# Performance work log

Measured on AMD Instinct MI355X. Metric: run time of the kernel, lower is better.

The kernel has to match this reference:

```python
import jax, jax.numpy as jnp
import numpy as np
from jax import lax

BSZ, BEAM, VOCAB, D = 32, 4, 50257, 1024
MAXLEN = 64
L = MAXLEN + 2            # tokens buffer length (bos + maxlen+1 slots)
SLEN = MAXLEN + 1         # scores buffer length
PAD, EOS, UNK = 1, 2, 3
TEMP = 1.0
LEN_PEN = 1.0
UNK_PEN = 0.0
NEG = jnp.float32(-1e9)   # stand-in for -inf (safe for grads)


def setup_inputs() -> dict:
    key = jax.random.key(0)
    k1, k2, k3 = jax.random.split(key, 3)
    # 0.02 scaling keeps logits in a realistic range
    emb = jax.random.normal(k1, (VOCAB, D), jnp.float32) * 0.02
    W_out = jax.random.normal(k2, (D, VOCAB), jnp.float32) * 0.02
    pos_emb = jax.random.normal(k3, (SLEN, D), jnp.float32) * 0.02
    return {"emb": emb, "W_out": W_out, "pos_emb": pos_emb}


def _decode(emb, W_out, pos_emb, tokens, step):
    # stand-in decoder: prev-token embedding + pos embedding -> vocab logits
    prev = lax.dynamic_index_in_dim(tokens, step, axis=1, keepdims=False)  # [bbsz]
    h = emb[prev] + pos_emb[step]                                          # [bbsz, D]
    lp = jax.nn.log_softmax((h @ W_out) / TEMP, axis=-1)                   # [bbsz, V]
    lp = lp.at[:, PAD].set(NEG)
    lp = lp.at[:, UNK].add(-UNK_PEN)
    return lp


def _beam_search(emb, W_out, pos_emb):
    bbsz = BSZ * BEAM
    tokens = jnp.full((bbsz, L), PAD, jnp.int32).at[:, 0].set(EOS)
    scores = jnp.zeros((bbsz, SLEN), jnp.float32)
    fin_tok = jnp.zeros((BSZ, BEAM, L), jnp.int32)
    fin_sc = jnp.full((BSZ, BEAM), NEG, jnp.float32)
    offsets = jnp.arange(2 * BEAM, dtype=jnp.int32)
    colL = jnp.arange(L)
    colS = jnp.arange(SLEN)
    barange = jnp.arange(BEAM)

    def step_fn(carry, step):
        tokens, scores, fin_tok, fin_sc = carry
        lp = _decode(emb, W_out, pos_emb, tokens, step).reshape(BSZ, BEAM, VOCAB)
        prev_sc = lax.dynamic_index_in_dim(scores, jnp.maximum(step - 1, 0), axis=1, keepdims=False)
        prev_sc = jnp.where(step == 0, 0.0, prev_sc).reshape(BSZ, BEAM)
        cum = lp + prev_sc[:, :, None]
        # step 0: only the first beam participates (fairseq BeamSearch.step)
        cum = jnp.where((step == 0) & (barange[None, :, None] > 0), NEG, cum)
        cand_sc, cand_flat = lax.top_k(cum.reshape(BSZ, BEAM * VOCAB), 2 * BEAM)
        cand_beam = cand_flat // VOCAB       # [BSZ, 2*BEAM]
        cand_tok = cand_flat % VOCAB
        tokens3 = tokens.reshape(BSZ, BEAM, L)
        # --- finalize eos hypotheses from the first BEAM candidates ---
        eos_mask_b = cand_tok[:, :BEAM] == EOS
        eos_norm = jnp.where(eos_mask_b, cand_sc[:, :BEAM] / (step + 1.0) ** LEN_PEN, NEG)
        eos_tok = jnp.take_along_axis(tokens3, cand_beam[:, :BEAM, None], axis=1)
        eos_tok = jnp.where(colL[None, None, :] == step + 1, EOS, eos_tok)
        all_sc = jnp.concatenate([fin_sc, eos_norm], axis=1)
        all_tok = jnp.concatenate([fin_tok, eos_tok], axis=1)
        fin_sc, sel = lax.top_k(all_sc, BEAM)
        fin_tok = jnp.take_along_axis(all_tok, sel[:, :, None], axis=1)
        # --- pick BEAM active (non-eos) hypotheses (smallest active_mask) ---
        eos_mask = (cand_tok == EOS).astype(jnp.int32)
        amask = eos_mask * (2 * BEAM) + offsets[None, :]
        _, active = lax.top_k(-amask, BEAM)
        act_beam = jnp.take_along_axis(cand_beam, active, axis=1)
        act_tok = jnp.take_along_axis(cand_tok, active, axis=1)
        act_sc = jnp.take_along_axis(cand_sc, active, axis=1)
        # --- reorder beams, append new token / score ---
        tokens3 = jnp.take_along_axis(tokens3, act_beam[:, :, None], axis=1)
        tokens3 = jnp.where(colL[None, None, :] == step + 1, act_tok[:, :, None], tokens3)
        scores3 = jnp.take_along_axis(scores.reshape(BSZ, BEAM, SLEN), act_beam[:, :, None], axis=1)
        scores3 = jnp.where(colS[None, None, :] == step, act_sc[:, :, None], scores3)
        return (tokens3.reshape(bbsz, L), scores3.reshape(bbsz, SLEN), fin_tok, fin_sc), None

    carry = (tokens, scores, fin_tok, fin_sc)
    (tokens, scores, fin_tok, fin_sc), _ = lax.scan(step_fn, carry, jnp.arange(MAXLEN))
    # --- final step: force EOS on every surviving beam (step == maxlen) ---
    lp = _decode(emb, W_out, pos_emb, tokens, MAXLEN)
    eos_sc = (scores[:, MAXLEN - 1] + lp[:, EOS]).reshape(BSZ, BEAM) / (MAXLEN + 1.0) ** LEN_PEN
    tokens3 = tokens.reshape(BSZ, BEAM, L)
    eos_tok = jnp.where(jnp.arange(L)[None, None, :] == MAXLEN + 1, EOS, tokens3)
    all_sc = jnp.concatenate([fin_sc, eos_sc], axis=1)
    all_tok = jnp.concatenate([fin_tok, eos_tok], axis=1)
    fin_sc, sel = lax.top_k(all_sc, BEAM)
    fin_tok = jnp.take_along_axis(all_tok, sel[:, :, None], axis=1)
    return fin_tok, fin_sc


def reference(emb, W_out, pos_emb):
    # returns (finalized tokens [BSZ, BEAM, L] int32, normalized scores [BSZ, BEAM] f32)
    return _beam_search(emb, W_out, pos_emb)
```

## Files before the change

kernel.cpp:

```cpp
#include <hip/hip_runtime.h>
#include <cstdint>
#include <cstddef>

#define VOCAB_N 50257
#define NPAD    50304
#define DIM     1024
#define BSZ_N   32
#define BEAM_N  4
#define BB      128
#define L_N     66
#define SLEN_N  65
#define MAXLEN_N 64
#define PAD_T   1
#define EOS_T   2
#define NEGV    (-1e9f)
#define SENTV   (-3.402823466e38f)
#define PW_BLOCK 128

typedef unsigned long long u64;
typedef __attribute__((ext_vector_type(8))) _Float16 f16x8;
typedef __attribute__((ext_vector_type(4))) _Float16 f16x4;
typedef __attribute__((ext_vector_type(4))) float f32x4;

__device__ __constant__ int QLO[4] = {0, 12560, 25128, 37688};
__device__ __constant__ int QHI[4] = {12560, 25128, 37688, 50257};

struct PWTree {
    int nleaf, nint, maxlev, root;
    int lstart[256], lnum[256], lslot[256];
    int eL[256], eR[256], eD[256];
    int lvl[32];
};

constexpr PWTree build_tree(int start, int n0) {
    PWTree t{};
    int fs[64] = {}, fn[64] = {}, fstt[64] = {}, fls[64] = {}, fll[64] = {};
    int tL[256] = {}, tR[256] = {}, tD[256] = {}, tLev[256] = {};
    int sp = 0, lc = 0, nc = 0, cnt = 0;
    fs[0] = start; fn[0] = n0; fstt[0] = 0; sp = 1;
    int retslot = -1, retlev = 0;
    while (sp > 0) {
        const int n = fn[sp - 1], s = fs[sp - 1], st = fstt[sp - 1];
        if (n <= PW_BLOCK) {
            t.lstart[lc] = s; t.lnum[lc] = n; t.lslot[lc] = cnt;
            retslot = cnt; retlev = 0; ++cnt; ++lc; --sp; continue;
        }
        int L = (n >> 1); L -= (L & 7);
        if (st == 0)      { fstt[sp - 1] = 1; fs[sp] = s;     fn[sp] = L;     fstt[sp] = 0; ++sp; }
        else if (st == 1) { fls[sp - 1] = retslot; fll[sp - 1] = retlev; fstt[sp - 1] = 2;
                            fs[sp] = s + L; fn[sp] = n - L; fstt[sp] = 0; ++sp; }
        else {
            const int lv = (fll[sp - 1] > retlev ? fll[sp - 1] : retlev) + 1;
            tL[nc] = fls[sp - 1]; tR[nc] = retslot; tD[nc] = cnt; tLev[nc] = lv;
            retslot = cnt; retlev = lv; ++cnt; ++nc; --sp;
        }
    }
    int maxlev = 0;
    for (int j = 0; j < nc; ++j) if (tLev[j] > maxlev) maxlev = tLev[j];
    int cl[40] = {};
    for (int j = 0; j < nc; ++j) cl[tLev[j]]++;
    int acc = 0;
    for (int v = 1; v <= maxlev; ++v) { t.lvl[v] = acc; acc += cl[v]; }
    t.lvl[maxlev + 1] = acc;
    int pos[40] = {};
    for (int v = 1; v <= maxlev; ++v) pos[v] = t.lvl[v];
    for (int j = 0; j < nc; ++j) {
        const int v = tLev[j]; const int p = pos[v]++;
        t.eL[p] = tL[j]; t.eR[p] = tR[j]; t.eD[p] = tD[j];
    }
    t.nleaf = lc; t.nint = nc; t.maxlev = maxlev; t.root = retslot;
    return t;
}

__device__ constexpr PWTree g_q0 = build_tree(0, 12560);
__device__ constexpr PWTree g_q1 = build_tree(12560, 12568);
__device__ constexpr PWTree g_q2 = build_tree(25128, 12560);
__device__ constexpr PWTree g_q3 = build_tree(37688, 12569);

__device__ __forceinline__ unsigned sortable_f32(float x) {
    unsigned u = __float_as_uint(x);
    return (u & 0x80000000u) ? ~u : (u | 0x80000000u);
}
__device__ __forceinline__ float unsort_f32(unsigned s) {
    unsigned u = (s & 0x80000000u) ? (s & 0x7fffffffu) : ~s;
    return __uint_as_float(u);
}

__global__ void k_init(int* __restrict__ tokens, float* __restrict__ scores,
                       int* __restrict__ fin_tok, float* __restrict__ fin_sc,
                       unsigned* __restrict__ rmax_u) {
    int i = blockIdx.x * blockDim.x + threadIdx.x;
    int st = gridDim.x * blockDim.x;
    for (int k = i; k < BB * L_N; k += st) tokens[k] = ((k % L_N) == 0) ? EOS_T : PAD_T;
    for (int k = i; k < BB * SLEN_N; k += st) scores[k] = 0.f;
    for (int k = i; k < BB * L_N; k += st) fin_tok[k] = 0;
    for (int k = i; k < BB; k += st) { fin_sc[k] = NEGV; rmax_u[k] = 0u; }
}

__device__ __forceinline__ void split2(float x, _Float16& h0, _Float16& h1) {
    const float xs = x * 4096.f;
    h0 = (_Float16)xs;
    const float r = xs - (float)h0;
    h1 = (_Float16)r;
}

__global__ __launch_bounds__(256) void k_wsplit(const float* __restrict__ W,
                                                _Float16* __restrict__ Wsp) {
    __shared__ __align__(16) _Float16 B[2][64][40];
    const int bid = blockIdx.x;
    const int ct = bid % 786, kt = bid / 786;
    const int n0 = ct * 64, k0 = kt * 32;
    const int tid = threadIdx.x;
    const int c = tid & 63, kk = tid >> 6;
#pragma unroll
    for (int j = 0; j < 8; ++j) {
        const int k = kk * 8 + j;
        float wv = 0.f;
        if (n0 + c < VOCAB_N) wv = W[(size_t)(k0 + k) * VOCAB_N + n0 + c];
        _Float16 b0, b1;
        split2(wv, b0, b1);
        B[0][c][k] = b0; B[1][c][k] = b1;
    }
    __syncthreads();
    const int g = tid & 3, cc = (tid >> 2) & 63;
#pragma unroll
    for (int p = 0; p < 2; ++p)
        *(f16x8*)&Wsp[((size_t)p * NPAD + n0 + cc) * 1024 + k0 + g * 8] =
            *(const f16x8*)&B[p][cc][g * 8];
}

__global__ __launch_bounds__(256) void k_hsplit(const float* __restrict__ emb,
                                                const float* __restrict__ pos_emb,
                                                const int* __restrict__ tokens,
                                                _Float16* __restrict__ Hsp, int step) {
    const int row = blockIdx.x;
    const int tid = threadIdx.x;
    const int tok = tokens[row * L_N + step];
    const float4 e = *(const float4*)(emb + (size_t)tok * DIM + tid * 4);
    const float4 p = *(const float4*)(pos_emb + (size_t)step * DIM + tid * 4);
    const float hv[4] = {e.x + p.x, e.y + p.y, e.z + p.z, e.w + p.w};
    f16x4 o0, o1;
#pragma unroll
    for (int d = 0; d < 4; ++d) {
        _Float16 a0, a1;
        split2(hv[d], a0, a1);
        o0[d] = a0; o1[d] = a1;
    }
    *(f16x4*)&Hsp[(size_t)0 * 131072 + row * 1024 + tid * 4] = o0;
    *(f16x4*)&Hsp[(size_t)1 * 131072 + row * 1024 + tid * 4] = o1;
}

__global__ __launch_bounds__(512) void k_gemm_fast(const _Float16* __restrict__ Wsp,
                                                   const _Float16* __restrict__ Hsp,
                                                   float* __restrict__ logits,
                                                   unsigned* __restrict__ rmax_u) {
    __shared__ __align__(16) _Float16 Ha[2][128][40];
    __shared__ __align__(16) _Float16 Wb[2][128][40];
    __shared__ unsigned smax[128];
    const int tid = threadIdx.x;
    const int n0 = blockIdx.x * 128;
    const int lane = tid & 63, wid = tid >> 6;
    const int la = lane & 15, g = lane >> 4;
    const int wr = wid >> 1, wc = wid & 1;
    const int sg = tid & 3, sidx = (tid >> 2) & 127;

    if (tid < 128) smax[tid] = 0u;

    f32x4 acc[2][4];
#pragma unroll
    for (int mf = 0; mf < 2; ++mf)
#pragma unroll
        for (int nf = 0; nf < 4; ++nf)
#pragma unroll
            for (int j = 0; j < 4; ++j) acc[mf][nf][j] = 0.f;

    const _Float16* H0 = Hsp;
    const _Float16* H1 = Hsp + 131072;
    const _Float16* W0 = Wsp;
    const _Float16* W1 = Wsp + (size_t)NPAD * 1024;
    const size_t hoff = (size_t)sidx * 1024 + sg * 8;
    const size_t woff = (size_t)(n0 + sidx) * 1024 + sg * 8;

    f16x8 rH0 = *(const f16x8*)&H0[hoff];
    f16x8 rH1 = *(const f16x8*)&H1[hoff];
    f16x8 rW0 = *(const f16x8*)&W0[woff];
    f16x8 rW1 = *(const f16x8*)&W1[woff];

    for (int t = 0; t < 32; ++t) {
        *(f16x8*)&Ha[0][sidx][sg * 8] = rH0;
        *(f16x8*)&Ha[1][sidx][sg * 8] = rH1;
        *(f16x8*)&Wb[0][sidx][sg * 8] = rW0;
        *(f16x8*)&Wb[1][sidx][sg * 8] = rW1;
        __syncthreads();
        if (t + 1 < 32) {
            const int k0 = (t + 1) * 32;
            rH0 = *(const f16x8*)&H0[hoff + k0];
            rH1 = *(const f16x8*)&H1[hoff + k0];
            rW0 = *(const f16x8*)&W0[woff + k0];
            rW1 = *(const f16x8*)&W1[woff + k0];
        }
        f16x8 a[2][2];
#pragma unroll
        for (int mf = 0; mf < 2; ++mf) {
            a[mf][0] = *(const f16x8*)&Ha[0][wr * 32 + mf * 16 + la][g * 8];
            a[mf][1] = *(const f16x8*)&Ha[1][wr * 32 + mf * 16 + la][g * 8];
        }
#pragma unroll
        for (int nf = 0; nf < 4; ++nf) {
            const int c = wc * 64 + nf * 16 + la;
            const f16x8 b0 = *(const f16x8*)&Wb[0][c][g * 8];
            const f16x8 b1 = *(const f16x8*)&Wb[1][c][g * 8];
#pragma unroll
            for (int mf = 0; mf < 2; ++mf) {
                f32x4 cc = acc[mf][nf];
                cc = __builtin_amdgcn_mfma_f32_16x16x32_f16(a[mf][0], b0, cc, 0, 0, 0);
                cc = __builtin_amdgcn_mfma_f32_16x16x32_f16(a[mf][0], b1, cc, 0, 0, 0);
                cc = __builtin_amdgcn_mfma_f32_16x16x32_f16(a[mf][1], b0, cc, 0, 0, 0);
                acc[mf][nf] = cc;
            }
        }
        __syncthreads();
    }

#pragma unroll
    for (int mf = 0; mf < 2; ++mf) {
        const int row = wr * 32 + mf * 16 + g * 4;
        float rmx[4] = {SENTV, SENTV, SENTV, SENTV};
#pragma unroll
        for (int nf = 0; nf < 4; ++nf) {
            const int col = n0 + wc * 64 + nf * 16 + la;
#pragma unroll
            for (int j = 0; j < 4; ++j) {
                const float v = acc[mf][nf][j] * 0x1p-24f;
                logits[(size_t)(row + j) * NPAD + col] = v;
                rmx[j] = fmaxf(rmx[j], v);
            }
        }
#pragma unroll
        for (int j = 0; j < 4; ++j) {
            float v = rmx[j];
            v = fmaxf(v, __shfl_xor(v, 1, 64));
            v = fmaxf(v, __shfl_xor(v, 2, 64));
            v = fmaxf(v, __shfl_xor(v, 4, 64));
            v = fmaxf(v, __shfl_xor(v, 8, 64));
            if (la == 0) atomicMax(&smax[row + j], sortable_f32(v));
        }
    }
    __syncthreads();
    if (tid < 128) atomicMax(&rmax_u[tid], smax[tid]);
}

#define KT 32
__global__ __launch_bounds__(512) void k_gemm_slow(const float* __restrict__ W,
                                                   const float* __restrict__ emb,
                                                   const float* __restrict__ pos_emb,
                                                   const int* __restrict__ tokens,
                                                   float* __restrict__ logits,
                                                   unsigned* __restrict__ rmax_u, int step) {
    __shared__ __align__(16) _Float16 Ha[2][128][40];
    __shared__ __align__(16) _Float16 Wb[2][128][40];
    __shared__ unsigned smax[128];
    const int tid = threadIdx.x;
    const int n0 = blockIdx.x * 128;
    const bool full = (n0 + 128 <= VOCAB_N);
    const int lane = tid & 63, wid = tid >> 6;
    const int wr = wid >> 1, wc = wid & 1;
    const int la = lane & 15, g = lane >> 4;
    const int hrow = tid & 127, hkq = tid >> 7;
    const int tokH = tokens[hrow * L_N + step];
    const float* eprow = emb + (size_t)tokH * DIM;
    const float* pprow = pos_emb + (size_t)step * DIM;
    const int wcq = tid & 31, wk = tid >> 5;

    if (tid < 128) smax[tid] = 0u;

    f32x4 acc[2][4];
#pragma unroll
    for (int mf = 0; mf < 2; ++mf)
#pragma unroll
        for (int nf = 0; nf < 4; ++nf)
#pragma unroll
            for (int j = 0; j < 4; ++j) acc[mf][nf][j] = 0.f;

    for (int k0 = 0; k0 < DIM; k0 += KT) {
#pragma unroll
        for (int d = 0; d < 4; ++d) {
            const int c = wcq + 32 * d;
#pragma unroll
            for (int qq = 0; qq < 2; ++qq) {
                const int kk = wk + 16 * qq;
                float wv = 0.f;
                if (full || (n0 + c < VOCAB_N))
                    wv = W[(size_t)(k0 + kk) * VOCAB_N + n0 + c];
                _Float16 b0, b1;
                split2(wv, b0, b1);
                Wb[0][c][kk] = b0;
                Wb[1][c][kk] = b1;
            }
        }
#pragma unroll
        for (int qq = 0; qq < 2; ++qq) {
            const int kq = hkq + 4 * qq;
            const float4 e0 = *(const float4*)(eprow + k0 + kq * 4);
            const float4 p0 = *(const float4*)(pprow + k0 + kq * 4);
            const float hv[4] = {e0.x + p0.x, e0.y + p0.y, e0.z + p0.z, e0.w + p0.w};
            f16x4 o0, o1;
#pragma unroll
            for (int d = 0; d < 4; ++d) {
                _Float16 a0, a1;
                split2(hv[d], a0, a1);
                o0[d] = a0; o1[d] = a1;
            }
            *(f16x4*)&Ha[0][hrow][kq * 4] = o0;
            *(f16x4*)&Ha[1][hrow][kq * 4] = o1;
        }
        __syncthreads();
        f16x8 af[2][2];
#pragma unroll
        for (int mf = 0; mf < 2; ++mf)
#pragma unroll
            for (int p = 0; p < 2; ++p)
                af[mf][p] = *(const f16x8*)&Ha[p][wr * 32 + mf * 16 + la][g * 8];
#pragma unroll
        for (int nf = 0; nf < 4; ++nf) {
            const int c = wc * 64 + nf * 16 + la;
            const f16x8 b0 = *(const f16x8*)&Wb[0][c][g * 8];
            const f16x8 b1 = *(const f16x8*)&Wb[1][c][g * 8];
#pragma unroll
            for (int mf = 0; mf < 2; ++mf) {
                f32x4 cc = acc[mf][nf];
                cc = __builtin_amdgcn_mfma_f32_16x16x32_f16(af[mf][0], b0, cc, 0, 0, 0);
                cc = __builtin_amdgcn_mfma_f32_16x16x32_f16(af[mf][0], b1, cc, 0, 0, 0);
                cc = __builtin_amdgcn_mfma_f32_16x16x32_f16(af[mf][1], b0, cc, 0, 0, 0);
                acc[mf][nf] = cc;
            }
        }
        __syncthreads();
    }
#pragma unroll
    for (int mf = 0; mf < 2; ++mf) {
        const int row = wr * 32 + mf * 16 + g * 4;
        float rmx[4] = {SENTV, SENTV, SENTV, SENTV};
#pragma unroll
        for (int nf = 0; nf < 4; ++nf) {
            const int col = n0 + wc * 64 + nf * 16 + la;
#pragma unroll
            for (int j = 0; j < 4; ++j) {
                const float v = acc[mf][nf][j] * 0x1p-24f;
                logits[(size_t)(row + j) * NPAD + col] = v;
                rmx[j] = fmaxf(rmx[j], v);
            }
        }
#pragma unroll
        for (int j = 0; j < 4; ++j) {
            float v = rmx[j];
            v = fmaxf(v, __shfl_xor(v, 1, 64));
            v = fmaxf(v, __shfl_xor(v, 2, 64));
            v = fmaxf(v, __shfl_xor(v, 4, 64));
            v = fmaxf(v, __shfl_xor(v, 8, 64));
            if (la == 0) atomicMax(&smax[row + j], sortable_f32(v));
        }
    }
    __syncthreads();
    if (tid < 128) atomicMax(&rmax_u[tid], smax[tid]);
}

__device__ __forceinline__ u64 pack_key(float x, int tk) {
    return ((u64)sortable_f32(x) << 32) | (unsigned)(VOCAB_N - tk);
}
__device__ __forceinline__ void insk16(u64 k, u64 lst[16]) {
#pragma unroll
    for (int p = 0; p < 16; ++p) {
        if (k > lst[p]) { u64 o = lst[p]; lst[p] = k; k = o; }
    }
}
__device__ __forceinline__ u64 wave_max_u64(u64 v) {
#pragma unroll
    for (int o = 32; o > 0; o >>= 1) {
        u64 w = __shfl_xor(v, o, 64);
        if (w > v) v = w;
    }
    return v;
}

#define RT2 256
__global__ __launch_bounds__(RT2) void k_scanexp(const float* __restrict__ logits,
                                                 const unsigned* __restrict__ rmax_u,
                                                 u64* __restrict__ htop,
                                                 float* __restrict__ qsum) {
    const int hb = blockIdx.x;
    const int row = hb >> 2, q = hb & 3;
    const int tid = threadIdx.x;
    const int lane = tid & 63, wid = tid >> 6;
    const float* x = logits + (size_t)row * NPAD;
    const int lo = QLO[q], hi = QHI[q];
    const float mrow = unsort_f32(rmax_u[row]);

    u64 lst[16];
#pragma unroll
    for (int p = 0; p < 16; ++p) lst[p] = 0ULL;
    for (int v = lo + tid * 4; v + 3 < hi; v += RT2 * 4) {
        const float4 t = *(const float4*)(x + v);
        const float va[4] = {t.x, t.y, t.z, t.w};
#pragma unroll
        for (int u = 0; u < 4; ++u) {
            const int tk = v + u;
            if (tk == PAD_T) continue;
            const u64 key = pack_key(va[u], tk);
            if (key > lst[15]) insk16(key, lst);
        }
    }
    if (q == 3 && tid == 0) {
        const int tk = VOCAB_N - 1;
        const u64 key = pack_key(x[tk], tk);
        if (key > lst[15]) insk16(key, lst);
    }

    __shared__ u64 wtop[4][16];
    for (int pass = 0; pass < 16; ++pass) {
        const u64 cand = lst[0];
        const u64 mx = wave_max_u64(cand);
        const u64 ball = __ballot(cand == mx);
        const int first = __ffsll((u64)ball) - 1;
        if (lane == first) {
#pragma unroll
            for (int p = 0; p < 15; ++p) lst[p] = lst[p + 1];
            lst[15] = 0ULL;
        }
        if (lane == 0) wtop[wid][pass] = mx;
    }
    __syncthreads();

    __shared__ u64 sfin[16];
    if (tid < 64) {
        const u64 mine = wtop[tid >> 4][tid & 15];
        bool taken = false;
        for (int pass = 0; pass < 16; ++pass) {
            const u64 cand = taken ? 0ULL : mine;
            const u64 mx = wave_max_u64(cand);
            const u64 ball = __ballot(cand == mx);
            const int first = __ffsll((u64)ball) - 1;
            if (tid == first) taken = true;
            if (tid == 0) sfin[pass] = mx;
        }
    }

    const PWTree& T = (q == 0) ? g_q0 : (q == 1) ? g_q1 : (q == 2) ? g_q2 : g_q3;
    __shared__ float slot[512];
    for (int leaf = tid; leaf < T.nleaf; leaf += RT2) {
        const int s = T.lstart[leaf];
        const int n = T.lnum[leaf];
        float res;
        if (n < 8) {
            res = 0.f;
            for (int i = 0; i < n; ++i) res += expf(x[s + i] - mrow);
        } else {
            float r0 = expf(x[s + 0] - mrow), r1 = expf(x[s + 1] - mrow);
            float r2 = expf(x[s + 2] - mrow), r3 = expf(x[s + 3] - mrow);
            float r4 = expf(x[s + 4] - mrow), r5 = expf(x[s + 5] - mrow);
            float r6 = expf(x[s + 6] - mrow), r7 = expf(x[s + 7] - mrow);
            int i = 8;
            const int lim = n - (n & 7);
            for (; i < lim; i += 8) {
                r0 += expf(x[s + i + 0] - mrow); r1 += expf(x[s + i + 1] - mrow);
                r2 += expf(x[s + i + 2] - mrow); r3 += expf(x[s + i + 3] - mrow);
                r4 += expf(x[s + i + 4] - mrow); r5 += expf(x[s + i + 5] - mrow);
                r6 += expf(x[s + i + 6] - mrow); r7 += expf(x[s + i + 7] - mrow);
            }
            res = ((r0 + r1) + (r2 + r3)) + ((r4 + r5) + (r6 + r7));
            for (; i < n; ++i) res += expf(x[s + i] - mrow);
        }
        slot[T.lslot[leaf]] = res;
    }
    __syncthreads();
    for (int lev = 1; lev <= T.maxlev; ++lev) {
        for (int j = T.lvl[lev] + tid; j < T.lvl[lev + 1]; j += RT2)
            slot[T.eD[j]] = slot[T.eL[j]] + slot[T.eR[j]];
        __syncthreads();
    }
    if (tid == 0) qsum[hb] = slot[T.root];
    if (tid < 16) htop[hb * 16 + tid] = sfin[tid];
}

__global__ __launch_bounds__(256) void k_beam(const u64* __restrict__ htop,
                                              unsigned* __restrict__ rmax_u,
                                              const float* __restrict__ qsum,
                                              int* __restrict__ tokens,
                                              float* __restrict__ scores,
                                              int* __restrict__ fin_tok,
                                              float* __restrict__ fin_sc,
                                              int step) {
    const int sent = blockIdx.x;
    const int tid = threadIdx.x;
    const int rN = (step == 0) ? 1 : BEAM_N;

    __shared__ u64 keys[4][64];
    for (int e = tid; e < 256; e += 256) {
        const int r = e >> 6, i = e & 63;
        keys[r][i] = htop[((sent * BEAM_N + r) * 4 + (i >> 4)) * 16 + (i & 15)];
    }
    __syncthreads();

    __shared__ u64 merged[4][16];
    if (tid < 4) {
        int ia[4] = {0, 0, 0, 0};
        for (int o = 0; o < 16; ++o) {
            u64 best = 0ULL; int bq = 0;
#pragma unroll
            for (int qq = 0; qq < 4; ++qq) {
                const u64 h = (ia[qq] < 16) ? keys[tid][qq * 16 + ia[qq]] : 0ULL;
                if (h > best) { best = h; bq = qq; }
            }
            merged[tid][o] = best; ia[bq]++;
        }
    }
    __syncthreads();

    __shared__ float bval[64]; __shared__ int bflat[64];
    if (tid < 16 * rN) {
        const int r = tid >> 4, j = tid & 15;
        const int row = sent * BEAM_N + r;
        const float rm = unsort_f32(rmax_u[row]);
        const float rl = (float)log((double)((qsum[row * 4] + qsum[row * 4 + 1]) +
                                             (qsum[row * 4 + 2] + qsum[row * 4 + 3])));
        const float prev = (step == 0) ? 0.f : scores[row * SLEN_N + step - 1];
        const u64 k = merged[r][j];
        const float xv = unsort_f32((unsigned)(k >> 32));
        const int   tk = VOCAB_N - (int)(k & 0xFFFFFFFFu);
        bval[tid]  = ((xv - rm) - rl) + prev;
        bflat[tid] = r * VOCAB_N + tk;
    }
    __syncthreads();
    __shared__ float cand_sc[8]; __shared__ int cand_flat[8];
    if (tid == 0) {
        const int nC = 16 * rN;
        for (int pass = 0; pass < 8; ++pass) {
            float bv = SENTV; int bi = 0x7fffffff; int bs = -1;
            for (int k = 0; k < nC; ++k) {
                const float v = bval[k]; const int ix = bflat[k];
                if (v > bv || (v == bv && ix < bi)) { bv = v; bi = ix; bs = k; }
            }
            cand_sc[pass] = bv; cand_flat[pass] = bi;
            bval[bs] = SENTV; bflat[bs] = 0x7fffffff;
        }
    }
    __syncthreads();

    __shared__ int   cur_tok[BEAM_N * L_N];
    __shared__ int   cur_fin[BEAM_N * L_N];
    __shared__ float cur_sc[BEAM_N * SLEN_N];
    for (int e = tid; e < BEAM_N * L_N; e += 256) {
        cur_tok[e] = tokens[sent * (BEAM_N * L_N) + e];
        cur_fin[e] = fin_tok[sent * (BEAM_N * L_N) + e];
    }
    for (int e = tid; e < BEAM_N * SLEN_N; e += 256)
        cur_sc[e] = scores[sent * (BEAM_N * SLEN_N) + e];
    __syncthreads();

    __shared__ int   tmp_fin[BEAM_N * L_N];
    __shared__ int   tmp_tok[BEAM_N * L_N];
    __shared__ float tmp_sc[BEAM_N * SLEN_N];
    __shared__ float nfin_s[BEAM_N];
    if (tid == 0) {
        int cb[8], ct[8];
#pragma unroll
        for (int j = 0; j < 8; ++j) {
            cb[j] = cand_flat[j] / VOCAB_N;
            ct[j] = cand_flat[j] % VOCAB_N;
        }
        float allsc[8];
#pragma unroll
        for (int j = 0; j < 4; ++j) allsc[j] = fin_sc[sent * BEAM_N + j];
#pragma unroll
        for (int j = 0; j < 4; ++j)
            allsc[4 + j] = (ct[j] == EOS_T) ? (cand_sc[j] / (float)(step + 1)) : NEGV;
        int fsel[4]; float nfin[4];
        bool used[8] = {false,false,false,false,false,false,false,false};
#pragma unroll
        for (int b = 0; b < 4; ++b) {
            int best = -1; float bvv = 0.f;
#pragma unroll
            for (int j = 0; j < 8; ++j) {
                if (used[j]) continue;
                if (best < 0 || allsc[j] > bvv) { best = j; bvv = allsc[j]; }
            }
            used[best] = true; fsel[b] = best; nfin[b] = bvv;
        }
#pragma unroll
        for (int b = 0; b < 4; ++b) {
            const int s = fsel[b];
            if (s < 4) {
                for (int p = 0; p < L_N; ++p) tmp_fin[b * L_N + p] = cur_fin[s * L_N + p];
            } else {
                const int bm = cb[s - 4];
                for (int p = 0; p < L_N; ++p)
                    tmp_fin[b * L_N + p] = (p == step + 1) ? EOS_T : cur_tok[bm * L_N + p];
            }
        }
        int ab[4], atk[4]; float asc[4]; int na = 0;
#pragma unroll
        for (int j = 0; j < 8; ++j) {
            if (na < 4 && ct[j] != EOS_T) { ab[na] = cb[j]; atk[na] = ct[j]; asc[na] = cand_sc[j]; ++na; }
        }
#pragma unroll
        for (int b = 0; b < 4; ++b) {
            const int bm = ab[b];
            for (int p = 0; p < L_N; ++p)
                tmp_tok[b * L_N + p] = (p == step + 1) ? atk[b] : cur_tok[bm * L_N + p];
            for (int p = 0; p < SLEN_N; ++p)
                tmp_sc[b * SLEN_N + p] = (p == step) ? asc[b] : cur_sc[bm * SLEN_N + p];
        }
#pragma unroll
        for (int b = 0; b < 4; ++b) nfin_s[b] = nfin[b];
    }
    __syncthreads();

    for (int e = tid; e < BEAM_N * L_N; e += 256) {
        fin_tok[sent * (BEAM_N * L_N) + e] = tmp_fin[e];
        tokens[sent * (BEAM_N * L_N) + e]  = tmp_tok[e];
    }
    for (int e = tid; e < BEAM_N * SLEN_N; e += 256)
        scores[sent * (BEAM_N * SLEN_N) + e] = tmp_sc[e];
    if (tid < 4) {
        fin_sc[sent * BEAM_N + tid] = nfin_s[tid];
        rmax_u[sent * BEAM_N + tid] = 0u;
    }
}

__global__ __launch_bounds__(256) void k_final(const float* __restrict__ logits,
                                               const unsigned* __restrict__ rmax_u,
                                               const float* __restrict__ qsum,
                                               const int* __restrict__ tokens,
                                               const float* __restrict__ scores,
                                               const int* __restrict__ fin_tok,
                                               const float* __restrict__ fin_sc,
                                               float* __restrict__ out) {
    const int sent = blockIdx.x;
    const int tid = threadIdx.x;
    __shared__ int fsel_s[4]; __shared__ float nfin_s[4];
    if (tid == 0) {
        float allsc[8];
#pragma unroll
        for (int r = 0; r < 4; ++r) {
            const int row = sent * BEAM_N + r;
            const float rm = unsort_f32(rmax_u[row]);
            const float rl = (float)log((double)((qsum[row * 4] + qsum[row * 4 + 1]) +
                                                 (qsum[row * 4 + 2] + qsum[row * 4 + 3])));
            const float lpE = ((logits[(size_t)row * NPAD + EOS_T] - rm) - rl);
            allsc[r] = fin_sc[sent * BEAM_N + r];
            allsc[4 + r] = (scores[row * SLEN_N + (MAXLEN_N - 1)] + lpE) / 65.0f;
        }
        bool used[8] = {false,false,false,false,false,false,false,false};
#pragma unroll
        for (int b = 0; b < 4; ++b) {
            int best = -1; float bvv = 0.f;
#pragma unroll
            for (int j = 0; j < 8; ++j) {
                if (used[j]) continue;
                if (best < 0 || allsc[j] > bvv) { best = j; bvv = allsc[j]; }
            }
            used[best] = true; fsel_s[b] = best; nfin_s[b] = bvv;
        }
    }
    __syncthreads();
    for (int e = tid; e < BEAM_N * L_N; e += 256) {
        const int b = e / L_N, p = e % L_N;
        const int s = fsel_s[b]; int valt;
        if (s < 4) {
            valt = fin_tok[(sent * BEAM_N + s) * L_N + p];
        } else {
            const int r = s - 4;
            valt = (p == MAXLEN_N + 1) ? EOS_T : tokens[(sent * BEAM_N + r) * L_N + p];
        }
        out[(size_t)(sent * BEAM_N + b) * L_N + p] = (float)valt;
    }
    if (tid < 4) out[BSZ_N * BEAM_N * L_N + sent * BEAM_N + tid] = nfin_s[tid];
}

extern "C" void kernel_launch(void* const* d_in, const int* in_sizes, int n_in,
                              void* d_out, int out_size, void* d_ws, size_t ws_size,
                              hipStream_t stream) {
    const float* emb = (const float*)d_in[0];
    const float* W   = (const float*)d_in[1];
    const float* pos = (const float*)d_in[2];
    float* out = (float*)d_out;

    char* w = (char*)d_ws;
    size_t off = 0;
    auto alloc = [&](size_t bytes) { void* p = w + off; off += (bytes + 15) & ~(size_t)15; return p; };
    float*    logits = (float*)alloc((size_t)BB * NPAD * 4);
    unsigned* rmax_u = (unsigned*)alloc(BB * 4);
    float*    qsum   = (float*)alloc(BB * 4 * 4);
    u64*      htop   = (u64*)alloc((size_t)BB * 4 * 16 * 8);
    int*      tokens = (int*)alloc(BB * L_N * 4);
    float*    scores = (float*)alloc(BB * SLEN_N * 4);
    int*      ftok   = (int*)alloc(BB * L_N * 4);
    float*    fsc    = (float*)alloc(BB * 4);
    _Float16* Wsp    = (_Float16*)alloc((size_t)2 * NPAD * 1024 * 2);
    _Float16* Hsp    = (_Float16*)alloc((size_t)2 * 128 * 1024 * 2);
    const bool fast = (off <= ws_size);

    k_init<<<32, 256, 0, stream>>>(tokens, scores, ftok, fsc, rmax_u);
    if (fast) k_wsplit<<<786 * 32, 256, 0, stream>>>(W, Wsp);
    for (int s = 0; s < MAXLEN_N; ++s) {
        if (fast) {
            k_hsplit<<<128, 256, 0, stream>>>(emb, pos, tokens, Hsp, s);
            k_gemm_fast<<<NPAD / 128, 512, 0, stream>>>(Wsp, Hsp, logits, rmax_u);
        } else {
            k_gemm_slow<<<NPAD / 128, 512, 0, stream>>>(W, emb, pos, tokens, logits, rmax_u, s);
        }
        k_scanexp<<<BB * 4, RT2, 0, stream>>>(logits, rmax_u, htop, qsum);
        k_beam<<<BSZ_N, 256, 0, stream>>>(htop, rmax_u, qsum, tokens, scores, ftok, fsc, s);
    }
    if (fast) {
        k_hsplit<<<128, 256, 0, stream>>>(emb, pos, tokens, Hsp, MAXLEN_N);
        k_gemm_fast<<<NPAD / 128, 512, 0, stream>>>(Wsp, Hsp, logits, rmax_u);
    } else {
        k_gemm_slow<<<NPAD / 128, 512, 0, stream>>>(W, emb, pos, tokens, logits, rmax_u, MAXLEN_N);
    }
    k_scanexp<<<BB * 4, RT2, 0, stream>>>(logits, rmax_u, htop, qsum);
    k_final<<<BSZ_N, 256, 0, stream>>>(logits, rmax_u, qsum, tokens, scores, ftok, fsc, out);
}
```

Before: 11.81 ms.

## Tile split W/H buffers by k-chunk and fuse next-step H split into beam kernel

Changes the split fp16 W and H buffers into a k-tiled layout ([kt][part][row][32]), so each GEMM k-step loads one contiguous 512-thread chunk instead of rows strided by 1024 elements. The wsplit kernel writes directly from registers, with no shared-memory transpose or barrier. The per-step hsplit launch is removed, and k_beam now computes the next step's embedding plus position split for its own rows. This cuts one kernel launch per step and improves load coalescing in the GEMM. In exchange k_beam gets extra tail work, and the wsplit stores become narrower and scattered.

```diff
diff --git a/kernel.cpp b/kernel.cpp
--- a/kernel.cpp
+++ b/kernel.cpp
@@ -104,29 +104,26 @@
     h1 = (_Float16)r;
 }
 
+
 __global__ __launch_bounds__(256) void k_wsplit(const float* __restrict__ W,
                                                 _Float16* __restrict__ Wsp) {
-    __shared__ __align__(16) _Float16 B[2][64][40];
     const int bid = blockIdx.x;
     const int ct = bid % 786, kt = bid / 786;
     const int n0 = ct * 64, k0 = kt * 32;
     const int tid = threadIdx.x;
-    const int c = tid & 63, kk = tid >> 6;
+    const int c = tid & 63, kk4 = tid >> 6;
+    _Float16 v0[8], v1[8];
 #pragma unroll
     for (int j = 0; j < 8; ++j) {
-        const int k = kk * 8 + j;
+        const int k = kk4 * 8 + j;
         float wv = 0.f;
         if (n0 + c < VOCAB_N) wv = W[(size_t)(k0 + k) * VOCAB_N + n0 + c];
-        _Float16 b0, b1;
-        split2(wv, b0, b1);
-        B[0][c][k] = b0; B[1][c][k] = b1;
-    }
-    __syncthreads();
-    const int g = tid & 3, cc = (tid >> 2) & 63;
-#pragma unroll
-    for (int p = 0; p < 2; ++p)
-        *(f16x8*)&Wsp[((size_t)p * NPAD + n0 + cc) * 1024 + k0 + g * 8] =
-            *(const f16x8*)&B[p][cc][g * 8];
+        split2(wv, v0[j], v1[j]);
+    }
+    const size_t base0 = ((size_t)(kt * 2 + 0) * NPAD + n0 + c) * 32 + kk4 * 8;
+    const size_t base1 = ((size_t)(kt * 2 + 1) * NPAD + n0 + c) * 32 + kk4 * 8;
+    *(f16x8*)&Wsp[base0] = *(f16x8*)v0;
+    *(f16x8*)&Wsp[base1] = *(f16x8*)v1;
 }
 
 __global__ __launch_bounds__(256) void k_hsplit(const float* __restrict__ emb,
@@ -136,8 +133,10 @@
     const int row = blockIdx.x;
     const int tid = threadIdx.x;
     const int tok = tokens[row * L_N + step];
-    const float4 e = *(const float4*)(emb + (size_t)tok * DIM + tid * 4);
-    const float4 p = *(const float4*)(pos_emb + (size_t)step * DIM + tid * 4);
+    const int k4 = tid * 4;
+    const int kt = k4 >> 5, kk = k4 & 31;
+    const float4 e = *(const float4*)(emb + (size_t)tok * DIM + k4);
+    const float4 p = *(const float4*)(pos_emb + (size_t)step * DIM + k4);
     const float hv[4] = {e.x + p.x, e.y + p.y, e.z + p.z, e.w + p.w};
     f16x4 o0, o1;
 #pragma unroll
@@ -146,8 +145,8 @@
         split2(hv[d], a0, a1);
         o0[d] = a0; o1[d] = a1;
     }
-    *(f16x4*)&Hsp[(size_t)0 * 131072 + row * 1024 + tid * 4] = o0;
-    *(f16x4*)&Hsp[(size_t)1 * 131072 + row * 1024 + tid * 4] = o1;
+    *(f16x4*)&Hsp[((size_t)(kt * 2 + 0) * 128 + row) * 32 + kk] = o0;
+    *(f16x4*)&Hsp[((size_t)(kt * 2 + 1) * 128 + row) * 32 + kk] = o1;
 }
 
 __global__ __launch_bounds__(512) void k_gemm_fast(const _Float16* __restrict__ Wsp,
@@ -162,7 +161,7 @@
     const int lane = tid & 63, wid = tid >> 6;
     const int la = lane & 15, g = lane >> 4;
     const int wr = wid >> 1, wc = wid & 1;
-    const int sg = tid & 3, sidx = (tid >> 2) & 127;
+    const int sidx = tid >> 2, sg = tid & 3;
 
     if (tid < 128) smax[tid] = 0u;
 
@@ -174,17 +173,14 @@
 #pragma unroll
             for (int j = 0; j < 4; ++j) acc[mf][nf][j] = 0.f;
 
-    const _Float16* H0 = Hsp;
-    const _Float16* H1 = Hsp + 131072;
-    const _Float16* W0 = Wsp;
-    const _Float16* W1 = Wsp + (size_t)NPAD * 1024;
-    const size_t hoff = (size_t)sidx * 1024 + sg * 8;
-    const size_t woff = (size_t)(n0 + sidx) * 1024 + sg * 8;
-
-    f16x8 rH0 = *(const f16x8*)&H0[hoff];
-    f16x8 rH1 = *(const f16x8*)&H1[hoff];
-    f16x8 rW0 = *(const f16x8*)&W0[woff];
-    f16x8 rW1 = *(const f16x8*)&W1[woff];
+    const size_t WT = (size_t)2 * NPAD * 32;
+    const size_t wbase = (size_t)n0 * 32 + tid * 8;
+    const size_t hbase = (size_t)tid * 8;
+
+    f16x8 rH0 = *(const f16x8*)&Hsp[hbase];
+    f16x8 rH1 = *(const f16x8*)&Hsp[4096 + hbase];
+    f16x8 rW0 = *(const f16x8*)&Wsp[wbase];
+    f16x8 rW1 = *(const f16x8*)&Wsp[(size_t)NPAD * 32 + wbase];
 
     for (int t = 0; t < 32; ++t) {
         *(f16x8*)&Ha[0][sidx][sg * 8] = rH0;
@@ -193,11 +189,12 @@
         *(f16x8*)&Wb[1][sidx][sg * 8] = rW1;
         __syncthreads();
         if (t + 1 < 32) {
-            const int k0 = (t + 1) * 32;
-            rH0 = *(const f16x8*)&H0[hoff + k0];
-            rH1 = *(const f16x8*)&H1[hoff + k0];
-            rW0 = *(const f16x8*)&W0[woff + k0];
-            rW1 = *(const f16x8*)&W1[woff + k0];
+            const size_t ho = (size_t)(t + 1) * 8192;
+            const size_t wo = (size_t)(t + 1) * WT;
+            rH0 = *(const f16x8*)&Hsp[ho + hbase];
+            rH1 = *(const f16x8*)&Hsp[ho + 4096 + hbase];
+            rW0 = *(const f16x8*)&Wsp[wo + wbase];
+            rW1 = *(const f16x8*)&Wsp[wo + (size_t)NPAD * 32 + wbase];
         }
         f16x8 a[2][2];
 #pragma unroll
@@ -489,6 +486,9 @@
                                               float* __restrict__ scores,
                                               int* __restrict__ fin_tok,
                                               float* __restrict__ fin_sc,
+                                              const float* __restrict__ emb,
+                                              const float* __restrict__ pos_emb,
+                                              _Float16* __restrict__ Hsp,
                                               int step) {
     const int sent = blockIdx.x;
     const int tid = threadIdx.x;
@@ -624,6 +624,33 @@
     if (tid < 4) {
         fin_sc[sent * BEAM_N + tid] = nfin_s[tid];
         rmax_u[sent * BEAM_N + tid] = 0u;
+    }
+
+    {
+        const int nstep = step + 1;
+        const int r = tid >> 6;
+        const int row = sent * BEAM_N + r;
+        const int tok = tmp_tok[r * L_N + nstep];
+        const int kb = (tid & 63) * 16;
+        const int kt = kb >> 5, kk0 = kb & 31;
+        const float* ep = emb + (size_t)tok * DIM + kb;
+        const float* pp = pos_emb + (size_t)nstep * DIM + kb;
+        _Float16 v0[16], v1[16];
+#pragma unroll
+        for (int jj = 0; jj < 4; ++jj) {
+            const float4 e = *(const float4*)(ep + jj * 4);
+            const float4 p = *(const float4*)(pp + jj * 4);
+            const float hv[4] = {e.x + p.x, e.y + p.y, e.z + p.z, e.w + p.w};
+#pragma unroll
+            for (int d = 0; d < 4; ++d)
+                split2(hv[d], v0[jj * 4 + d], v1[jj * 4 + d]);
+        }
+        _Float16* d0 = &Hsp[((size_t)(kt * 2 + 0) * 128 + row) * 32 + kk0];
+        _Float16* d1 = &Hsp[((size_t)(kt * 2 + 1) * 128 + row) * 32 + kk0];
+        *(f16x8*)d0       = *(f16x8*)&v0[0];
+        *(f16x8*)(d0 + 8) = *(f16x8*)&v0[8];
+        *(f16x8*)d1       = *(f16x8*)&v1[0];
+        *(f16x8*)(d1 + 8) = *(f16x8*)&v1[8];
     }
 }
 
@@ -701,19 +728,21 @@
     const bool fast = (off <= ws_size);
 
     k_init<<<32, 256, 0, stream>>>(tokens, scores, ftok, fsc, rmax_u);
-    if (fast) k_wsplit<<<786 * 32, 256, 0, stream>>>(W, Wsp);
+    if (fast) {
+        k_wsplit<<<786 * 32, 256, 0, stream>>>(W, Wsp);
+        k_hsplit<<<128, 256, 0, stream>>>(emb, pos, tokens, Hsp, 0);
+    }
     for (int s = 0; s < MAXLEN_N; ++s) {
         if (fast) {
-            k_hsplit<<<128, 256, 0, stream>>>(emb, pos, tokens, Hsp, s);
             k_gemm_fast<<<NPAD / 128, 512, 0, stream>>>(Wsp, Hsp, logits, rmax_u);
         } else {
             k_gemm_slow<<<NPAD / 128, 512, 0, stream>>>(W, emb, pos, tokens, logits, rmax_u, s);
         }
         k_scanexp<<<BB * 4, RT2, 0, stream>>>(logits, rmax_u, htop, qsum);
-        k_beam<<<BSZ_N, 256, 0, stream>>>(htop, rmax_u, qsum, tokens, scores, ftok, fsc, s);
+        k_beam<<<BSZ_N, 256, 0, stream>>>(htop, rmax_u, qsum, tokens, scores, ftok, fsc,
+                                          emb, pos, Hsp, s);
     }
     if (fast) {
-        k_hsplit<<<128, 256, 0, stream>>>(emb, pos, tokens, Hsp, MAXLEN_N);
         k_gemm_fast<<<NPAD / 128, 512, 0, stream>>>(Wsp, Hsp, logits, rmax_u);
     } else {
         k_gemm_slow<<<NPAD / 128, 512, 0, stream>>>(W, emb, pos, tokens, logits, rmax_u, MAXLEN_N);
```

Measured after the change: 11.35 ms. 1.04x faster.
